# Kernel optimization log

Hardware: AMD Instinct MI355X
Metric: run time of the kernel (lower is better)

## Reference

```python
import jax, jax.numpy as jnp
import numpy as np

DIM = 1024
NUM_HEADS = 16
HEAD_DIM = DIM // NUM_HEADS
SCALE = HEAD_DIM ** -0.5


def setup_inputs() -> dict:
    key = jax.random.key(0)
    k1, k2, k3, k4 = jax.random.split(key, 4)
    x = jax.random.normal(k1, (2, 2048, DIM), dtype=jnp.float32)
    # torch nn.Linear weights are [out, in]; init scale ~ 1/sqrt(in)
    s = DIM ** -0.5
    qkv_w = jax.random.normal(k2, (3 * DIM, DIM), dtype=jnp.float32) * s
    proj_w = jax.random.normal(k3, (DIM, DIM), dtype=jnp.float32) * s
    proj_b = jax.random.normal(k4, (DIM,), dtype=jnp.float32) * s
    return {"x": x, "qkv_w": qkv_w, "proj_w": proj_w, "proj_b": proj_b}


def reference(x, qkv_w, proj_w, proj_b):
    B, N, C = x.shape
    # qkv projection (no bias), split into q,k,v per head
    qkv = jnp.einsum('bnc,dc->bnd', x, qkv_w)               # [B,N,3C]
    qkv = qkv.reshape(B, N, 3, NUM_HEADS, HEAD_DIM)
    qkv = jnp.transpose(qkv, (2, 0, 3, 1, 4))               # [3,B,H,N,hd]
    q, k, v = qkv[0], qkv[1], qkv[2]
    attn = jnp.einsum('bhnd,bhmd->bhnm', q, k) * SCALE      # [B,H,N,N]
    attn = jax.nn.softmax(attn, axis=-1)
    out = jnp.einsum('bhnm,bhmd->bhnd', attn, v)            # [B,H,N,hd]
    out = jnp.transpose(out, (0, 2, 1, 3)).reshape(B, N, C)
    out = jnp.einsum('bnc,dc->bnd', out, proj_w) + proj_b
    return out
```

## Files before the change

### kernel.cpp

```cpp
#include <hip/hip_runtime.h>


typedef __bf16 bf16x8 __attribute__((ext_vector_type(8)));
typedef float f32x4 __attribute__((ext_vector_type(4)));

#if __has_builtin(__builtin_amdgcn_exp2f)
#define EXP2F(x) __builtin_amdgcn_exp2f(x)
#else
#define EXP2F(x) __expf((x)*0.69314718056f)
#endif

__device__ inline float bf2f(unsigned short u) {
    union { unsigned int i; float f; } v; v.i = ((unsigned int)u) << 16; return v.f;
}
__device__ inline unsigned short f2bf(float f) {
    union { float f; unsigned int i; } v; v.f = f;
    unsigned int u = v.i;
    return (unsigned short)((u + 0x7FFFu + ((u >> 16) & 1u)) >> 16);
}
__device__ inline unsigned short f2bf_trunc(float f) {
    union { float f; unsigned int i; } v; v.f = f;
    return (unsigned short)(v.i >> 16);
}
__device__ inline unsigned int pack2(float lo, float hi) {
    return (unsigned int)f2bf(lo) | ((unsigned int)f2bf(hi) << 16);
}
__device__ inline uint4 ld8(const unsigned short* p) { return *(const uint4*)p; }
__device__ inline uint4 ld8(const float* p) {
    float4 a = *(const float4*)p;
    float4 b = *(const float4*)(p + 4);
    uint4 r;
    r.x = pack2(a.x, a.y); r.y = pack2(a.z, a.w);
    r.z = pack2(b.x, b.y); r.w = pack2(b.z, b.w);
    return r;
}

__device__ inline void gld16(const unsigned short* g, unsigned short* l) {
    __builtin_amdgcn_global_load_lds(
        (const __attribute__((address_space(1))) unsigned int*)g,
        (__attribute__((address_space(3))) unsigned int*)l, 16, 0, 0);
}

__global__ __launch_bounds__(256) void cvt_kernel(const float* __restrict__ src,
                                                  unsigned short* __restrict__ dst,
                                                  int n8) {
    int i = blockIdx.x * blockDim.x + threadIdx.x;
    if (i < n8) *(uint4*)(dst + (size_t)i * 8) = ld8(src + (size_t)i * 8);
}

template <int WITH_BIAS, int OUT_F32, int MT>
__global__ __launch_bounds__(256) void gemm_fast(const unsigned short* __restrict__ A,
                                                 const unsigned short* __restrict__ W,
                                                 const float* __restrict__ bias,
                                                 void* __restrict__ Cv,
                                                 int M, int N, int K) {
    constexpr int BM = MT * 32;
    __shared__ unsigned short As[BM * 32];
    __shared__ unsigned short Bs[128 * 32];

    const int tid = threadIdx.x;
    const int wave = tid >> 6, lane = tid & 63;
    const int l15 = lane & 15, quad = lane >> 4;
    const int waveM = wave >> 1, waveN = wave & 1;
    const int bm = blockIdx.y * BM, bn = blockIdx.x * 128;
    const int lr = lane >> 2;
    const int lc = (lane & 3) * 8;

    f32x4 acc[MT][4];
    for (int i = 0; i < MT; i++)
        for (int j = 0; j < 4; j++) acc[i][j] = (f32x4){0.f, 0.f, 0.f, 0.f};

    for (int kb = 0; kb < K; kb += 32) {
        for (int p = 0; p < BM / 64; p++)
            gld16(A + (size_t)(bm + wave * (BM / 4) + p * 16 + lr) * K + kb + lc,
                  &As[(wave * (BM / 4) + p * 16) * 32]);
        gld16(W + (size_t)(bn + wave * 32 + lr) * K + kb + lc, &Bs[(wave * 32) * 32]);
        gld16(W + (size_t)(bn + wave * 32 + 16 + lr) * K + kb + lc, &Bs[(wave * 32 + 16) * 32]);
        __syncthreads();

        const int kcol = quad * 8;
        bf16x8 af[MT], bf[4];
        for (int mt = 0; mt < MT; mt++)
            af[mt] = *(const bf16x8*)(&As[(waveM * (MT * 16) + mt * 16 + l15) * 32 + kcol]);
        for (int nt = 0; nt < 4; nt++)
            bf[nt] = *(const bf16x8*)(&Bs[(waveN * 64 + nt * 16 + l15) * 32 + kcol]);
        for (int mt = 0; mt < MT; mt++)
            for (int nt = 0; nt < 4; nt++)
                acc[mt][nt] = __builtin_amdgcn_mfma_f32_16x16x32_bf16(af[mt], bf[nt], acc[mt][nt], 0, 0, 0);
        __syncthreads();
    }

    for (int mt = 0; mt < MT; mt++) {
        for (int nt = 0; nt < 4; nt++) {
            int col = bn + waveN * 64 + nt * 16 + l15;
            float bv = WITH_BIAS ? bias[col] : 0.f;
            for (int r = 0; r < 4; r++) {
                int row = bm + waveM * (MT * 16) + mt * 16 + quad * 4 + r;
                float v = acc[mt][nt][r] + bv;
                if (OUT_F32) ((float*)Cv)[(size_t)row * N + col] = v;
                else ((unsigned short*)Cv)[(size_t)row * N + col] = f2bf(v);
            }
        }
    }
}

template <int WITH_BIAS, int OUT_F32, typename TA, typename TW>
__global__ __launch_bounds__(256) void gemm_bt(const TA* __restrict__ A,
                                               const TW* __restrict__ W,
                                               const float* __restrict__ bias,
                                               void* __restrict__ Cv,
                                               int M, int N, int K) {
    const int LDSS = 40;
    __shared__ unsigned short As[128 * 40];
    __shared__ unsigned short Bs[128 * 40];

    const int tid = threadIdx.x;
    const int wave = tid >> 6, lane = tid & 63;
    const int l15 = lane & 15, quad = lane >> 4;
    const int waveM = wave >> 1, waveN = wave & 1;
    const int bm = blockIdx.y * 128, bn = blockIdx.x * 128;

    f32x4 acc[4][4];
    for (int i = 0; i < 4; i++)
        for (int j = 0; j < 4; j++) acc[i][j] = (f32x4){0.f, 0.f, 0.f, 0.f};

    for (int kb = 0; kb < K; kb += 32) {
        for (int c = tid; c < 512; c += 256) {
            int row = c >> 2, k0 = (c & 3) * 8;
            *(uint4*)(&As[row * LDSS + k0]) = ld8(A + (size_t)(bm + row) * K + kb + k0);
            *(uint4*)(&Bs[row * LDSS + k0]) = ld8(W + (size_t)(bn + row) * K + kb + k0);
        }
        __syncthreads();

        const int kcol = quad * 8;
        bf16x8 af[4], bf[4];
        for (int mt = 0; mt < 4; mt++)
            af[mt] = *(const bf16x8*)(&As[(waveM * 64 + mt * 16 + l15) * LDSS + kcol]);
        for (int nt = 0; nt < 4; nt++)
            bf[nt] = *(const bf16x8*)(&Bs[(waveN * 64 + nt * 16 + l15) * LDSS + kcol]);
        for (int mt = 0; mt < 4; mt++)
            for (int nt = 0; nt < 4; nt++)
                acc[mt][nt] = __builtin_amdgcn_mfma_f32_16x16x32_bf16(af[mt], bf[nt], acc[mt][nt], 0, 0, 0);
        __syncthreads();
    }

    for (int mt = 0; mt < 4; mt++) {
        for (int nt = 0; nt < 4; nt++) {
            int col = bn + waveN * 64 + nt * 16 + l15;
            float bv = WITH_BIAS ? bias[col] : 0.f;
            for (int r = 0; r < 4; r++) {
                int row = bm + waveM * 64 + mt * 16 + quad * 4 + r;
                float v = acc[mt][nt][r] + bv;
                if (OUT_F32) ((float*)Cv)[(size_t)row * N + col] = v;
                else ((unsigned short*)Cv)[(size_t)row * N + col] = f2bf(v);
            }
        }
    }
}

__global__ __launch_bounds__(512) void attn_kernel(const unsigned short* __restrict__ qkv,
                                                   unsigned short* __restrict__ y) {
    const int b = blockIdx.z, h = blockIdx.y;
    const int q0 = blockIdx.x * 128;
    const int tid = threadIdx.x;
    const int wave = tid >> 6, lane = tid & 63;
    const int l15 = lane & 15, quad = lane >> 4;

    const int QS = 72;
    const int PS = 68;
    __shared__ unsigned short QPs[128 * 68];
    __shared__ unsigned short Ks[64 * 72];
    __shared__ unsigned short Vt[64 * 72];

    const size_t bbase = (size_t)b * 2048;

    {
        int row = tid >> 2, k0 = (tid & 3) * 16;
        const unsigned short* src = qkv + (bbase + q0 + row) * 3072 + h * 64 + k0;
        for (int half = 0; half < 2; half++) {
            uint4 v = *(const uint4*)(src + half * 8);
            const unsigned short* pv = (const unsigned short*)&v;
            uint4 ov;
            unsigned int* po = (unsigned int*)&ov;
            for (int j = 0; j < 4; j++)
                po[j] = pack2(bf2f(pv[2 * j]) * 0.18033688f,
                              bf2f(pv[2 * j + 1]) * 0.18033688f);
            *(uint4*)(&QPs[row * PS + k0 + half * 8]) = ov;
        }
    }
    __syncthreads();
    bf16x8 aq0 = *(const bf16x8*)(&QPs[(wave * 16 + l15) * PS + quad * 8]);
    bf16x8 aq1 = *(const bf16x8*)(&QPs[(wave * 16 + l15) * PS + 32 + quad * 8]);

    bf16x8 vone;
    for (int j = 0; j < 8; j++) vone[j] = (__bf16)1.0f;

    f32x4 o[4], ol;
    for (int nt = 0; nt < 4; nt++) o[nt] = (f32x4){0.f, 0.f, 0.f, 0.f};
    ol = (f32x4){0.f, 0.f, 0.f, 0.f};

    for (int kb = 0; kb < 2048; kb += 64) {
        __syncthreads();

        {
            int row = tid >> 3, k0 = (tid & 7) * 8;
            uint4 vk = *(const uint4*)(qkv + (bbase + kb + row) * 3072 + h * 64 + 1024 + k0);
            *(uint4*)(&Ks[row * QS + k0]) = vk;
        }
        {
            int rp = tid >> 4, db = (tid & 15) * 4;
            const size_t r0 = (bbase + kb + 2 * rp) * 3072 + h * 64 + 2048 + db;
            uint2 v0 = *(const uint2*)(qkv + r0);
            uint2 v1 = *(const uint2*)(qkv + r0 + 3072);
            const unsigned short* p0 = (const unsigned short*)&v0;
            const unsigned short* p1 = (const unsigned short*)&v1;
            int sw = (db >> 3) & 3;
            int keysw = (2 * rp) ^ (sw << 4);
            for (int j = 0; j < 4; j++) {
                unsigned int w = (unsigned int)p0[j] | ((unsigned int)p1[j] << 16);
                *(unsigned int*)(&Vt[(db + j) * QS + keysw]) = w;
            }
        }
        __syncthreads();

        f32x4 s[4];
        for (int nt = 0; nt < 4; nt++) {
            bf16x8 bk0 = *(const bf16x8*)(&Ks[(nt * 16 + l15) * QS + quad * 8]);
            bf16x8 bk1 = *(const bf16x8*)(&Ks[(nt * 16 + l15) * QS + 32 + quad * 8]);
            f32x4 t = (f32x4){0.f, 0.f, 0.f, 0.f};
            t = __builtin_amdgcn_mfma_f32_16x16x32_bf16(aq0, bk0, t, 0, 0, 0);
            t = __builtin_amdgcn_mfma_f32_16x16x32_bf16(aq1, bk1, t, 0, 0, 0);
            s[nt] = t;
        }

        for (int nt = 0; nt < 4; nt++)
            for (int r = 0; r < 4; r++) {
                float p = EXP2F(s[nt][r] - 11.5415603f);
                QPs[(wave * 16 + quad * 4 + r) * PS + nt * 16 + l15] = f2bf_trunc(p);
            }

        bf16x8 ap0 = *(const bf16x8*)(&QPs[(wave * 16 + l15) * PS + quad * 8]);
        bf16x8 ap1 = *(const bf16x8*)(&QPs[(wave * 16 + l15) * PS + 32 + quad * 8]);
        for (int nt = 0; nt < 4; nt++) {
            int dd = nt * 16 + l15;
            int sw = (dd >> 3) & 3;
            bf16x8 bv0 = *(const bf16x8*)(&Vt[dd * QS + ((quad * 8) ^ (sw << 4))]);
            bf16x8 bv1 = *(const bf16x8*)(&Vt[dd * QS + ((32 + quad * 8) ^ (sw << 4))]);
            o[nt] = __builtin_amdgcn_mfma_f32_16x16x32_bf16(ap0, bv0, o[nt], 0, 0, 0);
            o[nt] = __builtin_amdgcn_mfma_f32_16x16x32_bf16(ap1, bv1, o[nt], 0, 0, 0);
        }
        ol = __builtin_amdgcn_mfma_f32_16x16x32_bf16(ap0, vone, ol, 0, 0, 0);
        ol = __builtin_amdgcn_mfma_f32_16x16x32_bf16(ap1, vone, ol, 0, 0, 0);
    }

    float rl[4];
    for (int r = 0; r < 4; r++) rl[r] = 1.0f / ol[r];
    for (int nt = 0; nt < 4; nt++)
        for (int r = 0; r < 4; r++) {
            int row = q0 + wave * 16 + quad * 4 + r;
            y[(bbase + row) * 1024 + h * 64 + nt * 16 + l15] = f2bf(o[nt][r] * rl[r]);
        }
}

extern "C" void kernel_launch(void* const* d_in, const int* in_sizes, int n_in,
                              void* d_out, int out_size, void* d_ws, size_t ws_size,
                              hipStream_t stream) {
    const float* x = (const float*)d_in[0];
    const float* qkv_w = (const float*)d_in[1];
    const float* proj_w = (const float*)d_in[2];
    const float* proj_b = (const float*)d_in[3];
    float* out = (float*)d_out;

    unsigned short* qkv = (unsigned short*)d_ws;
    unsigned short* slot2 = qkv + (size_t)4096 * 3072;

    const size_t FAST_WS = (size_t)40 * 1024 * 1024;
    if (ws_size >= FAST_WS) {
        unsigned short* xb = slot2;
        unsigned short* qwb = (unsigned short*)((char*)d_ws + 32 * 1024 * 1024);
        unsigned short* pwb = (unsigned short*)((char*)d_ws + 38 * 1024 * 1024);
        unsigned short* y = slot2;

        cvt_kernel<<<2048, 256, 0, stream>>>(x, xb, 4096 * 1024 / 8);
        cvt_kernel<<<1536, 256, 0, stream>>>(qkv_w, qwb, 3072 * 1024 / 8);
        cvt_kernel<<<512, 256, 0, stream>>>(proj_w, pwb, 1024 * 1024 / 8);

        gemm_fast<0, 0, 4><<<dim3(24, 32), dim3(256), 0, stream>>>(
            xb, qwb, nullptr, qkv, 4096, 3072, 1024);
        attn_kernel<<<dim3(16, 16, 2), dim3(512), 0, stream>>>(qkv, y);
        gemm_fast<1, 1, 2><<<dim3(8, 64), dim3(256), 0, stream>>>(
            y, pwb, proj_b, out, 4096, 1024, 1024);
    } else {
        unsigned short* y = slot2;
        gemm_bt<0, 0, float, float><<<dim3(24, 32), dim3(256), 0, stream>>>(
            x, qkv_w, nullptr, qkv, 4096, 3072, 1024);
        attn_kernel<<<dim3(16, 16, 2), dim3(512), 0, stream>>>(qkv, y);
        gemm_bt<1, 1, unsigned short, float><<<dim3(8, 32), dim3(256), 0, stream>>>(
            y, proj_w, proj_b, out, 4096, 1024, 1024);
    }
}
```

Measured before the change: 219.1 us.

## Prefetch K/V tiles into registers, use 128-key tiles, merge conversion kernels

The attention loop now loads the next 128-key K and V tile into registers while computing on the current one. Each loaded tile is processed as two 64-key chunks, which halves the number of barriers per key. The three fp32-to-bf16 conversion launches are merged into one kernel. The constant exponent offset is removed, which relies on the normalization cancelling it but adds some overflow risk for large scores.

New measurement: 196.7 us. -10.2%, faster.

```diff
diff --git a/kernel.cpp b/kernel.cpp
--- a/kernel.cpp
+++ b/kernel.cpp
@@ -41,11 +41,24 @@
         (__attribute__((address_space(3))) unsigned int*)l, 16, 0, 0);
 }
 
-__global__ __launch_bounds__(256) void cvt_kernel(const float* __restrict__ src,
-                                                  unsigned short* __restrict__ dst,
-                                                  int n8) {
+__global__ __launch_bounds__(256) void cvt3_kernel(const float* __restrict__ x,
+                                                   const float* __restrict__ qw,
+                                                   const float* __restrict__ pw,
+                                                   unsigned short* __restrict__ xb,
+                                                   unsigned short* __restrict__ qwb,
+                                                   unsigned short* __restrict__ pwb) {
     int i = blockIdx.x * blockDim.x + threadIdx.x;
-    if (i < n8) *(uint4*)(dst + (size_t)i * 8) = ld8(src + (size_t)i * 8);
+    const int NX = 4096 * 1024 / 8;
+    const int NQ = 3072 * 1024 / 8;
+    if (i < NX) {
+        *(uint4*)(xb + (size_t)i * 8) = ld8(x + (size_t)i * 8);
+    } else if (i < NX + NQ) {
+        int j = i - NX;
+        *(uint4*)(qwb + (size_t)j * 8) = ld8(qw + (size_t)j * 8);
+    } else {
+        int j = i - NX - NQ;
+        *(uint4*)(pwb + (size_t)j * 8) = ld8(pw + (size_t)j * 8);
+    }
 }
 
 template <int WITH_BIAS, int OUT_F32, int MT>
@@ -166,11 +179,12 @@
     const int wave = tid >> 6, lane = tid & 63;
     const int l15 = lane & 15, quad = lane >> 4;
 
-    const int QS = 72;
     const int PS = 68;
+    const int KS = 72;
+    const int VS = 136;
     __shared__ unsigned short QPs[128 * 68];
-    __shared__ unsigned short Ks[64 * 72];
-    __shared__ unsigned short Vt[64 * 72];
+    __shared__ unsigned short Ks[128 * 72];
+    __shared__ unsigned short Vt[64 * 136];
 
     const size_t bbase = (size_t)b * 2048;
 
@@ -199,58 +213,70 @@
     for (int nt = 0; nt < 4; nt++) o[nt] = (f32x4){0.f, 0.f, 0.f, 0.f};
     ol = (f32x4){0.f, 0.f, 0.f, 0.f};
 
-    for (int kb = 0; kb < 2048; kb += 64) {
-        __syncthreads();
-
+    const int krow = tid >> 2, kcol0 = (tid & 3) * 16;
+    const int vrp = tid >> 3, vdb = (tid & 7) * 8;
+    const int vsw = (tid & 7) & 3;
+    const int vkeysw = (2 * vrp) ^ (vsw << 4);
+    const unsigned short* kptr = qkv + (bbase + krow) * 3072 + h * 64 + 1024 + kcol0;
+    const unsigned short* vptr = qkv + (bbase + 2 * vrp) * 3072 + h * 64 + 2048 + vdb;
+
+    uint4 kA0 = *(const uint4*)(kptr);
+    uint4 kA1 = *(const uint4*)(kptr + 8);
+    uint4 vA0 = *(const uint4*)(vptr);
+    uint4 vA1 = *(const uint4*)(vptr + 3072);
+
+    for (int kb = 0; kb < 2048; kb += 128) {
+        __syncthreads();
+
+        *(uint4*)(&Ks[krow * KS + kcol0]) = kA0;
+        *(uint4*)(&Ks[krow * KS + kcol0 + 8]) = kA1;
         {
-            int row = tid >> 3, k0 = (tid & 7) * 8;
-            uint4 vk = *(const uint4*)(qkv + (bbase + kb + row) * 3072 + h * 64 + 1024 + k0);
-            *(uint4*)(&Ks[row * QS + k0]) = vk;
-        }
-        {
-            int rp = tid >> 4, db = (tid & 15) * 4;
-            const size_t r0 = (bbase + kb + 2 * rp) * 3072 + h * 64 + 2048 + db;
-            uint2 v0 = *(const uint2*)(qkv + r0);
-            uint2 v1 = *(const uint2*)(qkv + r0 + 3072);
-            const unsigned short* p0 = (const unsigned short*)&v0;
-            const unsigned short* p1 = (const unsigned short*)&v1;
-            int sw = (db >> 3) & 3;
-            int keysw = (2 * rp) ^ (sw << 4);
-            for (int j = 0; j < 4; j++) {
+            const unsigned short* p0 = (const unsigned short*)&vA0;
+            const unsigned short* p1 = (const unsigned short*)&vA1;
+            for (int j = 0; j < 8; j++) {
                 unsigned int w = (unsigned int)p0[j] | ((unsigned int)p1[j] << 16);
-                *(unsigned int*)(&Vt[(db + j) * QS + keysw]) = w;
-            }
-        }
-        __syncthreads();
-
-        f32x4 s[4];
-        for (int nt = 0; nt < 4; nt++) {
-            bf16x8 bk0 = *(const bf16x8*)(&Ks[(nt * 16 + l15) * QS + quad * 8]);
-            bf16x8 bk1 = *(const bf16x8*)(&Ks[(nt * 16 + l15) * QS + 32 + quad * 8]);
-            f32x4 t = (f32x4){0.f, 0.f, 0.f, 0.f};
-            t = __builtin_amdgcn_mfma_f32_16x16x32_bf16(aq0, bk0, t, 0, 0, 0);
-            t = __builtin_amdgcn_mfma_f32_16x16x32_bf16(aq1, bk1, t, 0, 0, 0);
-            s[nt] = t;
-        }
-
-        for (int nt = 0; nt < 4; nt++)
-            for (int r = 0; r < 4; r++) {
-                float p = EXP2F(s[nt][r] - 11.5415603f);
-                QPs[(wave * 16 + quad * 4 + r) * PS + nt * 16 + l15] = f2bf_trunc(p);
-            }
-
-        bf16x8 ap0 = *(const bf16x8*)(&QPs[(wave * 16 + l15) * PS + quad * 8]);
-        bf16x8 ap1 = *(const bf16x8*)(&QPs[(wave * 16 + l15) * PS + 32 + quad * 8]);
-        for (int nt = 0; nt < 4; nt++) {
-            int dd = nt * 16 + l15;
-            int sw = (dd >> 3) & 3;
-            bf16x8 bv0 = *(const bf16x8*)(&Vt[dd * QS + ((quad * 8) ^ (sw << 4))]);
-            bf16x8 bv1 = *(const bf16x8*)(&Vt[dd * QS + ((32 + quad * 8) ^ (sw << 4))]);
-            o[nt] = __builtin_amdgcn_mfma_f32_16x16x32_bf16(ap0, bv0, o[nt], 0, 0, 0);
-            o[nt] = __builtin_amdgcn_mfma_f32_16x16x32_bf16(ap1, bv1, o[nt], 0, 0, 0);
-        }
-        ol = __builtin_amdgcn_mfma_f32_16x16x32_bf16(ap0, vone, ol, 0, 0, 0);
-        ol = __builtin_amdgcn_mfma_f32_16x16x32_bf16(ap1, vone, ol, 0, 0, 0);
+                *(unsigned int*)(&Vt[(vdb + j) * VS + vkeysw]) = w;
+            }
+        }
+        __syncthreads();
+
+        int nkb = (kb + 128 < 2048) ? kb + 128 : 0;
+        size_t koff = (size_t)nkb * 3072;
+        kA0 = *(const uint4*)(kptr + koff);
+        kA1 = *(const uint4*)(kptr + koff + 8);
+        vA0 = *(const uint4*)(vptr + koff);
+        vA1 = *(const uint4*)(vptr + koff + 3072);
+
+        for (int c = 0; c < 2; c++) {
+            f32x4 s[4];
+            for (int nt = 0; nt < 4; nt++) {
+                const unsigned short* kr = &Ks[(c * 64 + nt * 16 + l15) * KS + quad * 8];
+                bf16x8 bk0 = *(const bf16x8*)(kr);
+                bf16x8 bk1 = *(const bf16x8*)(kr + 32);
+                f32x4 t = (f32x4){0.f, 0.f, 0.f, 0.f};
+                t = __builtin_amdgcn_mfma_f32_16x16x32_bf16(aq0, bk0, t, 0, 0, 0);
+                t = __builtin_amdgcn_mfma_f32_16x16x32_bf16(aq1, bk1, t, 0, 0, 0);
+                s[nt] = t;
+            }
+
+            for (int nt = 0; nt < 4; nt++)
+                for (int r = 0; r < 4; r++)
+                    QPs[(wave * 16 + quad * 4 + r) * PS + nt * 16 + l15] =
+                        f2bf_trunc(EXP2F(s[nt][r]));
+
+            bf16x8 ap0 = *(const bf16x8*)(&QPs[(wave * 16 + l15) * PS + quad * 8]);
+            bf16x8 ap1 = *(const bf16x8*)(&QPs[(wave * 16 + l15) * PS + 32 + quad * 8]);
+            for (int nt = 0; nt < 4; nt++) {
+                int dd = nt * 16 + l15;
+                int sw = (dd >> 3) & 3;
+                bf16x8 bv0 = *(const bf16x8*)(&Vt[dd * VS + ((c * 64 + quad * 8) ^ (sw << 4))]);
+                bf16x8 bv1 = *(const bf16x8*)(&Vt[dd * VS + ((c * 64 + 32 + quad * 8) ^ (sw << 4))]);
+                o[nt] = __builtin_amdgcn_mfma_f32_16x16x32_bf16(ap0, bv0, o[nt], 0, 0, 0);
+                o[nt] = __builtin_amdgcn_mfma_f32_16x16x32_bf16(ap1, bv1, o[nt], 0, 0, 0);
+            }
+            ol = __builtin_amdgcn_mfma_f32_16x16x32_bf16(ap0, vone, ol, 0, 0, 0);
+            ol = __builtin_amdgcn_mfma_f32_16x16x32_bf16(ap1, vone, ol, 0, 0, 0);
+        }
     }
 
     float rl[4];
@@ -281,9 +307,7 @@
         unsigned short* pwb = (unsigned short*)((char*)d_ws + 38 * 1024 * 1024);
         unsigned short* y = slot2;
 
-        cvt_kernel<<<2048, 256, 0, stream>>>(x, xb, 4096 * 1024 / 8);
-        cvt_kernel<<<1536, 256, 0, stream>>>(qkv_w, qwb, 3072 * 1024 / 8);
-        cvt_kernel<<<512, 256, 0, stream>>>(proj_w, pwb, 1024 * 1024 / 8);
+        cvt3_kernel<<<4096, 256, 0, stream>>>(x, qkv_w, proj_w, xb, qwb, pwb);
 
         gemm_fast<0, 0, 4><<<dim3(24, 32), dim3(256), 0, stream>>>(
             xb, qwb, nullptr, qkv, 4096, 3072, 1024);
```
